# Optimization experiments

Measured on AMD Instinct MI355X. Metric: run time of the kernel, lower is better.

## Reference

```python
import jax, jax.numpy as jnp
import numpy as np

D_MODEL = 1024
D_HIDDEN = 4096
NUM_EXPERTS = 8
K_ACTIVE = 2


def setup_inputs() -> dict:
    key = jax.random.key(0)
    ks = jax.random.split(key, 8)
    x = jax.random.normal(ks[0], (1, 2048, D_MODEL), dtype=jnp.float32)
    gate_w = jax.random.normal(ks[1], (D_MODEL, NUM_EXPERTS), dtype=jnp.float32) * 0.02
    gate_b = jnp.zeros((NUM_EXPERTS,), dtype=jnp.float32)
    w1 = jax.random.normal(ks[2], (NUM_EXPERTS, D_MODEL, D_HIDDEN), dtype=jnp.float32) * 0.02
    b1 = jnp.zeros((NUM_EXPERTS, D_HIDDEN), dtype=jnp.float32)
    w2 = jax.random.normal(ks[3], (NUM_EXPERTS, D_HIDDEN, D_MODEL), dtype=jnp.float32) * 0.02
    b2 = jnp.zeros((NUM_EXPERTS, D_MODEL), dtype=jnp.float32)
    return {"x": x, "gate_w": gate_w, "gate_b": gate_b,
            "w1": w1, "b1": b1, "w2": w2, "b2": b2}


def reference(x, gate_w, gate_b, w1, b1, w2, b2):
    B, S, D = x.shape
    xf = x.reshape(-1, D)                                    # [T, D]
    logits = xf @ gate_w + gate_b                            # [T, E]
    top_w, top_idx = jax.lax.top_k(logits, K_ACTIVE)         # [T, K]
    top_w = jax.nn.softmax(top_w, axis=-1)                   # softmax over selected experts
    # combine-weight per expert: sum over k slots of one-hot(idx) * weight -> [T, E]
    gates = jnp.sum(jax.nn.one_hot(top_idx, NUM_EXPERTS, dtype=xf.dtype) * top_w[..., None], axis=1)
    # expert FFN applied per expert (dropout is identity in eval): gelu is exact (erf), matching torch nn.GELU default
    h = jax.nn.gelu(jnp.einsum('td,edh->teh', xf, w1) + b1[None], approximate=False)  # [T, E, H]
    y = jnp.einsum('teh,ehd->ted', h, w2) + b2[None]         # [T, E, D]
    out = jnp.einsum('ted,te->td', y, gates)                 # weighted combine of selected experts
    return out.reshape(B, S, D)
```

## Files before the change

kernel.cpp:

```cpp
#include <hip/hip_runtime.h>
#include <stdint.h>

typedef unsigned short u16;
typedef __attribute__((ext_vector_type(8))) short s16x8;
typedef __attribute__((ext_vector_type(8))) u16  u16x8;
typedef __attribute__((ext_vector_type(4))) u16  u16x4;
typedef __attribute__((ext_vector_type(4))) float f32x4;

#define T_TOKENS 2048
#define DM 1024
#define DH 4096
#define NE 8
#define BK 64
#define PAD2 256
#define MAXS2 (T_TOKENS*2 + NE*PAD2)
#define RB1 (MAXS2/256)
#define RB2 (MAXS2/128)
#define BM 128
#define BN 128
#define MAXSLOTS (T_TOKENS*2 + NE*BM)
#define ROWBLK (MAXSLOTS/BM)

__device__ __forceinline__ u16 f2bf(float f) {
    union { float ff; uint32_t u; } v; v.ff = f;
    uint32_t r = v.u + 0x7fffu + ((v.u >> 16) & 1u);
    return (u16)(r >> 16);
}

#define GLOAD_LDS16(gsrc, ldst) \
    __builtin_amdgcn_global_load_lds((const __attribute__((address_space(1))) uint32_t*)(gsrc), \
                                     (__attribute__((address_space(3))) uint32_t*)(ldst), 16, 0, 0)

#define WAIT_VM8() asm volatile("s_waitcnt vmcnt(8)" ::: "memory")
#define WAIT_VM0() asm volatile("s_waitcnt vmcnt(0)" ::: "memory")

__global__ void k_convert(const float* __restrict__ x, u16* __restrict__ xbf,
                          int* __restrict__ ctrl) {
    int i = blockIdx.x * blockDim.x + threadIdx.x;
    const f32x4* xv = (const f32x4*)x;
    f32x4 a = xv[2*i], b = xv[2*i+1];
    u16x8 o;
    o[0]=f2bf(a[0]); o[1]=f2bf(a[1]); o[2]=f2bf(a[2]); o[3]=f2bf(a[3]);
    o[4]=f2bf(b[0]); o[5]=f2bf(b[1]); o[6]=f2bf(b[2]); o[7]=f2bf(b[3]);
    ((u16x8*)xbf)[i] = o;
    if (blockIdx.x == 0 && threadIdx.x < 32) ctrl[threadIdx.x] = 0;
}

__global__ void __launch_bounds__(256) k_transpose(const float* __restrict__ src,
                                                   u16* __restrict__ dst,
                                                   int K, int N, int nw0, int NW) {
    __shared__ float tile[64][65];
    const int e = blockIdx.z;
    const int n0 = nw0 + blockIdx.x * 64, k0 = blockIdx.y * 64;
    const float* s = src + (size_t)e * K * N;
    u16* d = dst + (size_t)e * K * NW;
    const int tx = threadIdx.x & 15, ty = threadIdx.x >> 4;
    #pragma unroll
    for (int j = 0; j < 4; ++j) {
        int r = ty * 4 + j;
        f32x4 v = *(const f32x4*)(s + (size_t)(k0 + r) * N + n0 + tx * 4);
        tile[r][tx*4+0] = v[0]; tile[r][tx*4+1] = v[1];
        tile[r][tx*4+2] = v[2]; tile[r][tx*4+3] = v[3];
    }
    __syncthreads();
    #pragma unroll
    for (int j = 0; j < 4; ++j) {
        int n = ty * 4 + j;
        u16x4 w;
        #pragma unroll
        for (int c = 0; c < 4; ++c) w[c] = f2bf(tile[tx*4+c][n]);
        *(u16x4*)(d + (size_t)(n0 - nw0 + n) * K + k0 + tx * 4) = w;
    }
}

__global__ void __launch_bounds__(64) k_gate(const float* __restrict__ x,
                                             const float* __restrict__ gw,
                                             const float* __restrict__ gb,
                                             int* __restrict__ cnt,
                                             int* __restrict__ tt_idx,
                                             float* __restrict__ tt_w) {
    const int t = blockIdx.x;
    const int lane = threadIdx.x;
    float acc[NE] = {0.f,0.f,0.f,0.f,0.f,0.f,0.f,0.f};
    const float* xr = x + (size_t)t * DM;
    #pragma unroll
    for (int c = 0; c < DM/64; ++c) {
        float xv = xr[lane + 64*c];
        const float* g = gw + (size_t)(lane + 64*c) * NE;
        #pragma unroll
        for (int e = 0; e < NE; ++e) acc[e] += xv * g[e];
    }
    #pragma unroll
    for (int e = 0; e < NE; ++e) {
        #pragma unroll
        for (int off = 32; off >= 1; off >>= 1)
            acc[e] += __shfl_xor(acc[e], off, 64);
    }
    if (lane == 0) {
        float l[NE];
        #pragma unroll
        for (int e = 0; e < NE; ++e) l[e] = acc[e] + gb[e];
        int i0 = 0;
        #pragma unroll
        for (int e = 1; e < NE; ++e) if (l[e] > l[i0]) i0 = e;
        int i1 = (i0 == 0) ? 1 : 0;
        #pragma unroll
        for (int e = 0; e < NE; ++e) if (e != i0 && l[e] > l[i1]) i1 = e;
        float m  = l[i0];
        float w0 = expf(l[i0] - m), w1 = expf(l[i1] - m);
        float s = w0 + w1; w0 /= s; w1 /= s;
        tt_idx[t*2] = i0; tt_idx[t*2+1] = i1;
        tt_w[t*2] = w0;  tt_w[t*2+1] = w1;
        atomicAdd(&cnt[i0], 1); atomicAdd(&cnt[i1], 1);
    }
}

__global__ void k_offsets(const int* __restrict__ cnt, int* __restrict__ fill,
                          int* __restrict__ off, int pad) {
    if (threadIdx.x == 0 && blockIdx.x == 0) {
        int a = 0;
        for (int e = 0; e < NE; ++e) {
            off[e] = a;
            a += (cnt[e] + pad - 1) / pad * pad;
            fill[e] = 0;
        }
        off[NE] = a;
    }
}

__global__ void k_scatter(const int* __restrict__ tt_idx, const float* __restrict__ tt_w,
                          const int* __restrict__ off, int* __restrict__ fill,
                          int* __restrict__ slot_token, float* __restrict__ slot_gate) {
    int t = blockIdx.x * blockDim.x + threadIdx.x;
    if (t >= T_TOKENS) return;
    #pragma unroll
    for (int k = 0; k < 2; ++k) {
        int e = tt_idx[t*2+k];
        int pos = off[e] + atomicAdd(&fill[e], 1);
        slot_token[pos] = t;
        slot_gate[pos]  = tt_w[t*2+k];
    }
}

__device__ __forceinline__ void mma64(const u16* As, const u16* Bs, int lane,
                                      int wr, int wc, f32x4 acc[4][4]) {
    #pragma unroll
    for (int ko = 0; ko < 2; ++ko) {
        s16x8 af[4], bfr[4];
        #pragma unroll
        for (int m = 0; m < 4; ++m) {
            int row = wr*64 + m*16 + (lane & 15);
            int sl = (ko*4 + (lane >> 4)) ^ (row & 7);
            af[m] = *(const s16x8*)&As[row*BK + sl*8];
        }
        #pragma unroll
        for (int n = 0; n < 4; ++n) {
            int col = wc*64 + n*16 + (lane & 15);
            int sl = (ko*4 + (lane >> 4)) ^ (col & 7);
            bfr[n] = *(const s16x8*)&Bs[col*BK + sl*8];
        }
        #pragma unroll
        for (int m = 0; m < 4; ++m)
            #pragma unroll
            for (int n = 0; n < 4; ++n)
                acc[m][n] = __builtin_amdgcn_mfma_f32_16x16x32_bf16(af[m], bfr[n], acc[m][n], 0, 0, 0);
    }
}

__device__ __forceinline__ void mma256(const u16* As, const u16* Bs, int lane,
                                       int wr, int wc, f32x4 acc[8][4]) {
    #pragma unroll
    for (int ko = 0; ko < 2; ++ko) {
        s16x8 af[8], bfr[4];
        #pragma unroll
        for (int m = 0; m < 8; ++m) {
            int row = wr*128 + m*16 + (lane & 15);
            int sl = (ko*4 + (lane >> 4)) ^ (row & 7);
            af[m] = *(const s16x8*)&As[row*BK + sl*8];
        }
        #pragma unroll
        for (int n = 0; n < 4; ++n) {
            int col = wc*64 + n*16 + (lane & 15);
            int sl = (ko*4 + (lane >> 4)) ^ (col & 7);
            bfr[n] = *(const s16x8*)&Bs[col*BK + sl*8];
        }
        #pragma unroll
        for (int m = 0; m < 8; ++m)
            #pragma unroll
            for (int n = 0; n < 4; ++n)
                acc[m][n] = __builtin_amdgcn_mfma_f32_16x16x32_bf16(af[m], bfr[n], acc[m][n], 0, 0, 0);
    }
}

__global__ void __launch_bounds__(512, 2) k_ffn1_256(
    const u16* __restrict__ xbf, const u16* __restrict__ wt,
    const float* __restrict__ b1, const int* __restrict__ slot_token,
    const int* __restrict__ off, u16* __restrict__ h, int cb0, int NW)
{
    __shared__ u16 As[2][256*BK];
    __shared__ u16 Bs[2][256*BK];
    const int rb = blockIdx.y, cbl = blockIdx.x;
    const int total = off[NE];
    const int r0 = rb * 256;
    if (r0 >= total) return;
    int e = 0;
    while (e < NE-1 && off[e+1] <= r0) e++;
    const u16* Bsrc = wt + (size_t)e * DM * NW;
    const float* be = b1 + (size_t)e * DH;
    const int colbase = (cb0 + cbl) * 256;

    const int tid = threadIdx.x;
    const int lane = tid & 63, wid = tid >> 6;
    const int wr = wid >> 2, wc = wid & 3;

    const u16* gA[4]; const u16* gB[4];
    #pragma unroll
    for (int i = 0; i < 4; ++i) {
        int row = wid*32 + i*8 + (lane >> 3);
        int g = (lane & 7) ^ (row & 7);
        int tok = slot_token[r0 + row];
        gA[i] = xbf + (size_t)tok * DM + g*8;
        gB[i] = Bsrc + (size_t)(cbl*256 + row) * DM + g*8;
    }

    f32x4 acc[8][4];
    #pragma unroll
    for (int m = 0; m < 8; ++m)
        #pragma unroll
        for (int n = 0; n < 4; ++n) acc[m][n] = (f32x4){0.f,0.f,0.f,0.f};

    #define STG1(buf, kt) do {                                                \
        _Pragma("unroll")                                                     \
        for (int i = 0; i < 4; ++i) {                                         \
            GLOAD_LDS16(gA[i] + (kt)*BK, &As[buf][(wid*32 + i*8)*BK]);        \
            GLOAD_LDS16(gB[i] + (kt)*BK, &Bs[buf][(wid*32 + i*8)*BK]);        \
        }                                                                     \
    } while (0)

    const int NT = DM / BK;
    STG1(0, 0);
    STG1(1, 1);
    #pragma unroll 1
    for (int kt = 0; kt < NT; ++kt) {
        if (kt + 1 < NT) WAIT_VM8(); else WAIT_VM0();
        __builtin_amdgcn_s_barrier();
        __builtin_amdgcn_s_setprio(1);
        mma256(As[kt & 1], Bs[kt & 1], lane, wr, wc, acc);
        __builtin_amdgcn_s_setprio(0);
        __builtin_amdgcn_s_barrier();
        if (kt + 2 < NT) STG1(kt & 1, kt + 2);
    }
    #undef STG1

    #pragma unroll
    for (int n = 0; n < 4; ++n) {
        int col = colbase + wc*64 + n*16 + (lane & 15);
        float bb = be[col];
        #pragma unroll
        for (int m = 0; m < 8; ++m) {
            int rbase = r0 + wr*128 + m*16 + (lane >> 4)*4;
            #pragma unroll
            for (int i = 0; i < 4; ++i) {
                float v = acc[m][n][i] + bb;
                float gv = 0.5f * v * (1.0f + erff(v * 0.70710678118654752f));
                h[(size_t)(rbase + i)*DH + col] = f2bf(gv);
            }
        }
    }
}

__global__ void __launch_bounds__(256) k_ffn2_b16(
    const u16* __restrict__ h, const u16* __restrict__ w2t,
    const float* __restrict__ b2, const int* __restrict__ slot_token,
    const float* __restrict__ slot_gate, const int* __restrict__ off,
    float* __restrict__ out)
{
    __shared__ u16 As[2][BM*BK];
    __shared__ u16 Bs[2][BN*BK];
    const int rb = blockIdx.y, cb = blockIdx.x;
    const int total = off[NE];
    const int r0 = rb * BM;
    if (r0 >= total) return;
    int e = 0;
    while (e < NE-1 && off[e+1] <= r0) e++;
    const u16* Bsrc = w2t + (size_t)e * DH * DM;
    const float* be = b2 + (size_t)e * DM;

    const int tid = threadIdx.x;
    const int lane = tid & 63, wid = tid >> 6;
    const int wr = wid >> 1, wc = wid & 1;

    const u16* gA[4]; const u16* gB[4];
    #pragma unroll
    for (int i = 0; i < 4; ++i) {
        int row = wid*32 + i*8 + (lane >> 3);
        int g = (lane & 7) ^ (row & 7);
        gA[i] = h + (size_t)(r0 + row) * DH + g*8;
        gB[i] = Bsrc + (size_t)(cb*BN + row) * DH + g*8;
    }

    f32x4 acc[4][4];
    #pragma unroll
    for (int m = 0; m < 4; ++m)
        #pragma unroll
        for (int n = 0; n < 4; ++n) acc[m][n] = (f32x4){0.f,0.f,0.f,0.f};

    #define STG2(buf, kt) do {                                                \
        _Pragma("unroll")                                                     \
        for (int i = 0; i < 4; ++i) {                                         \
            GLOAD_LDS16(gA[i] + (kt)*BK, &As[buf][(wid*32 + i*8)*BK]);        \
            GLOAD_LDS16(gB[i] + (kt)*BK, &Bs[buf][(wid*32 + i*8)*BK]);        \
        }                                                                     \
    } while (0)

    const int NT = DH / BK;
    STG2(0, 0);
    STG2(1, 1);
    #pragma unroll 1
    for (int kt = 0; kt < NT; ++kt) {
        if (kt + 1 < NT) WAIT_VM8(); else WAIT_VM0();
        __builtin_amdgcn_s_barrier();
        __builtin_amdgcn_s_setprio(1);
        mma64(As[kt & 1], Bs[kt & 1], lane, wr, wc, acc);
        __builtin_amdgcn_s_setprio(0);
        __builtin_amdgcn_s_barrier();
        if (kt + 2 < NT) STG2(kt & 1, kt + 2);
    }
    #undef STG2

    float bb[4];
    #pragma unroll
    for (int n = 0; n < 4; ++n) bb[n] = be[cb*BN + wc*64 + n*16 + (lane & 15)];
    #pragma unroll
    for (int m = 0; m < 4; ++m) {
        #pragma unroll
        for (int i = 0; i < 4; ++i) {
            int s = r0 + wr*64 + m*16 + (lane >> 4)*4 + i;
            int tok = slot_token[s];
            float g = slot_gate[s];
            if (g != 0.0f) {
                float* orow = out + (size_t)tok * DM + cb*BN + wc*64;
                #pragma unroll
                for (int n = 0; n < 4; ++n)
                    atomicAdd(orow + n*16 + (lane & 15), g * (acc[m][n][i] + bb[n]));
            }
        }
    }
}


__global__ void __launch_bounds__(256) k_ffn1_f32(
    const u16* __restrict__ xbf, const float* __restrict__ w1,
    const float* __restrict__ b1, const int* __restrict__ slot_token,
    const int* __restrict__ off, u16* __restrict__ h)
{
    __shared__ u16 As[BM*BK];
    __shared__ u16 Bs[BN*BK];
    const int rb = blockIdx.y, cb = blockIdx.x;
    const int total = off[NE];
    const int r0 = rb * BM;
    if (r0 >= total) return;
    int e = 0;
    while (e < NE-1 && off[e+1] <= r0) e++;
    const float* Bsrc = w1 + (size_t)e * DM * DH;
    const float* be   = b1 + (size_t)e * DH;

    const int tid = threadIdx.x;
    const int lane = tid & 63, wid = tid >> 6;
    const int wr = wid >> 1, wc = wid & 1;

    const u16* gA[4];
    #pragma unroll
    for (int i = 0; i < 4; ++i) {
        int row = wid*32 + i*8 + (lane >> 3);
        int g = (lane & 7) ^ (row & 7);
        int tok = slot_token[r0 + row];
        gA[i] = xbf + (size_t)tok * DM + g*8;
    }
    const int tc = tid & 31, tr = tid >> 5;
    const float* gB = Bsrc + (size_t)(tr*8) * DH + cb*BN + tc*4;

    f32x4 acc[4][4];
    #pragma unroll
    for (int m = 0; m < 4; ++m)
        #pragma unroll
        for (int n = 0; n < 4; ++n) acc[m][n] = (f32x4){0.f,0.f,0.f,0.f};

    for (int kt = 0; kt < DM/BK; ++kt) {
        #pragma unroll
        for (int i = 0; i < 4; ++i)
            GLOAD_LDS16(gA[i] + kt*BK, &As[(wid*32 + i*8)*BK]);
        f32x4 bv[8];
        #pragma unroll
        for (int j = 0; j < 8; ++j)
            bv[j] = *(const f32x4*)(gB + (size_t)(kt*BK + j) * DH);
        #pragma unroll
        for (int c = 0; c < 4; ++c) {
            int n = tc*4 + c;
            int sl = tr ^ (n & 7);
            s16x8 pk;
            #pragma unroll
            for (int j = 0; j < 8; ++j) pk[j] = (short)f2bf(bv[j][c]);
            *(s16x8*)&Bs[n*BK + sl*8] = pk;
        }
        __syncthreads();
        mma64(As, Bs, lane, wr, wc, acc);
        __syncthreads();
    }
    #pragma unroll
    for (int n = 0; n < 4; ++n) {
        int col = cb*BN + wc*64 + n*16 + (lane & 15);
        float bb = be[col];
        #pragma unroll
        for (int m = 0; m < 4; ++m) {
            int rbase = r0 + wr*64 + m*16 + (lane >> 4)*4;
            #pragma unroll
            for (int i = 0; i < 4; ++i) {
                float v = acc[m][n][i] + bb;
                float gv = 0.5f * v * (1.0f + erff(v * 0.70710678118654752f));
                h[(size_t)(rbase + i)*DH + col] = f2bf(gv);
            }
        }
    }
}

__global__ void __launch_bounds__(256) k_ffn2_f32(
    const u16* __restrict__ h, const float* __restrict__ w2,
    const float* __restrict__ b2, const int* __restrict__ slot_token,
    const float* __restrict__ slot_gate, const int* __restrict__ off,
    float* __restrict__ out)
{
    __shared__ u16 As[BM*BK];
    __shared__ u16 Bs[BN*BK];
    const int rb = blockIdx.y, cb = blockIdx.x;
    const int total = off[NE];
    const int r0 = rb * BM;
    if (r0 >= total) return;
    int e = 0;
    while (e < NE-1 && off[e+1] <= r0) e++;
    const float* Bsrc = w2 + (size_t)e * DH * DM;
    const float* be   = b2 + (size_t)e * DM;

    const int tid = threadIdx.x;
    const int lane = tid & 63, wid = tid >> 6;
    const int wr = wid >> 1, wc = wid & 1;

    const u16* gA[4];
    #pragma unroll
    for (int i = 0; i < 4; ++i) {
        int row = wid*32 + i*8 + (lane >> 3);
        int g = (lane & 7) ^ (row & 7);
        gA[i] = h + (size_t)(r0 + row) * DH + g*8;
    }
    const int tc = tid & 31, tr = tid >> 5;
    const float* gB = Bsrc + (size_t)(tr*8) * DM + cb*BN + tc*4;

    f32x4 acc[4][4];
    #pragma unroll
    for (int m = 0; m < 4; ++m)
        #pragma unroll
        for (int n = 0; n < 4; ++n) acc[m][n] = (f32x4){0.f,0.f,0.f,0.f};

    for (int kt = 0; kt < DH/BK; ++kt) {
        #pragma unroll
        for (int i = 0; i < 4; ++i)
            GLOAD_LDS16(gA[i] + kt*BK, &As[(wid*32 + i*8)*BK]);
        f32x4 bv[8];
        #pragma unroll
        for (int j = 0; j < 8; ++j)
            bv[j] = *(const f32x4*)(gB + (size_t)(kt*BK + j) * DM);
        #pragma unroll
        for (int c = 0; c < 4; ++c) {
            int n = tc*4 + c;
            int sl = tr ^ (n & 7);
            s16x8 pk;
            #pragma unroll
            for (int j = 0; j < 8; ++j) pk[j] = (short)f2bf(bv[j][c]);
            *(s16x8*)&Bs[n*BK + sl*8] = pk;
        }
        __syncthreads();
        mma64(As, Bs, lane, wr, wc, acc);
        __syncthreads();
    }
    float bb[4];
    #pragma unroll
    for (int n = 0; n < 4; ++n) bb[n] = be[cb*BN + wc*64 + n*16 + (lane & 15)];
    #pragma unroll
    for (int m = 0; m < 4; ++m) {
        #pragma unroll
        for (int i = 0; i < 4; ++i) {
            int s = r0 + wr*64 + m*16 + (lane >> 4)*4 + i;
            int tok = slot_token[s];
            float g = slot_gate[s];
            if (g != 0.0f) {
                float* orow = out + (size_t)tok * DM + cb*BN + wc*64;
                #pragma unroll
                for (int n = 0; n < 4; ++n)
                    atomicAdd(orow + n*16 + (lane & 15), g * (acc[m][n][i] + bb[n]));
            }
        }
    }
}

extern "C" void kernel_launch(void* const* d_in, const int* in_sizes, int n_in,
                              void* d_out, int out_size, void* d_ws, size_t ws_size,
                              hipStream_t stream)
{
    (void)in_sizes; (void)n_in; (void)out_size;
    const float* x  = (const float*)d_in[0];
    const float* gw = (const float*)d_in[1];
    const float* gb = (const float*)d_in[2];
    const float* w1 = (const float*)d_in[3];
    const float* b1 = (const float*)d_in[4];
    const float* w2 = (const float*)d_in[5];
    const float* b2 = (const float*)d_in[6];
    float* out = (float*)d_out;
    char* ws = (char*)d_ws;

    const size_t OFF_XBF = 0;
    const size_t OFF_H   = 4194304;
    const size_t OFF_ST  = OFF_H + (size_t)MAXS2 * DH * 2;
    const size_t OFF_SG  = OFF_ST + MAXS2 * 4;
    const size_t OFF_TI  = OFF_SG + MAXS2 * 4;
    const size_t OFF_TW  = OFF_TI + T_TOKENS * 2 * 4;
    const size_t OFF_CT  = OFF_TW + T_TOKENS * 2 * 4;
    const size_t OFF_WT  = (OFF_CT + 128 + 255) & ~(size_t)255;
    const size_t NEED_FULL = OFF_WT + (size_t)NE * DM * DH * 2;
    const size_t NEED_HALF = OFF_WT + (size_t)NE * DM * (DH/2) * 2;

    if (ws_size >= NEED_HALF) {
        u16*   xbf        = (u16*)(ws + OFF_XBF);
        u16*   h          = (u16*)(ws + OFF_H);
        int*   slot_token = (int*)(ws + OFF_ST);
        float* slot_gate  = (float*)(ws + OFF_SG);
        int*   tt_idx     = (int*)(ws + OFF_TI);
        float* tt_w       = (float*)(ws + OFF_TW);
        int*   ctrl       = (int*)(ws + OFF_CT);
        u16*   wt         = (u16*)(ws + OFF_WT);
        int* cnt = ctrl; int* fill = ctrl + 8; int* offs = ctrl + 16;
        const int full = (ws_size >= NEED_FULL);

        hipMemsetAsync(slot_token, 0, 2 * MAXS2 * 4, stream);
        hipMemsetAsync(out, 0, (size_t)T_TOKENS * DM * sizeof(float), stream);

        k_convert<<<(T_TOKENS*DM/8 + 255)/256, 256, 0, stream>>>(x, xbf, ctrl);
        k_gate<<<T_TOKENS, 64, 0, stream>>>(x, gw, gb, cnt, tt_idx, tt_w);
        k_offsets<<<1, 64, 0, stream>>>(cnt, fill, offs, PAD2);
        k_scatter<<<(T_TOKENS + 255)/256, 256, 0, stream>>>(tt_idx, tt_w, offs, fill,
                                                            slot_token, slot_gate);
        if (full) {
            k_transpose<<<dim3(DH/64, DM/64, NE), 256, 0, stream>>>(w1, wt, DM, DH, 0, DH);
            k_ffn1_256<<<dim3(DH/256, RB1), 512, 0, stream>>>(xbf, wt, b1, slot_token, offs, h, 0, DH);
        } else {
            k_transpose<<<dim3(DH/128, DM/64, NE), 256, 0, stream>>>(w1, wt, DM, DH, 0, DH/2);
            k_ffn1_256<<<dim3(DH/512, RB1), 512, 0, stream>>>(xbf, wt, b1, slot_token, offs, h, 0, DH/2);
            k_transpose<<<dim3(DH/128, DM/64, NE), 256, 0, stream>>>(w1, wt, DM, DH, DH/2, DH/2);
            k_ffn1_256<<<dim3(DH/512, RB1), 512, 0, stream>>>(xbf, wt, b1, slot_token, offs, h, DH/512, DH/2);
        }
        k_transpose<<<dim3(DM/64, DH/64, NE), 256, 0, stream>>>(w2, wt, DH, DM, 0, DM);
        k_ffn2_b16<<<dim3(DM/BN, RB2), 256, 0, stream>>>(h, wt, b2, slot_token, slot_gate, offs, out);
    } else {
        u16*   xbf        = (u16*)(ws);
        u16*   h          = (u16*)(ws + 4194304);
        int*   slot_token = (int*)(ws + 46137344);
        float* slot_gate  = (float*)(ws + 46157824);
        int*   tt_idx     = (int*)(ws + 46178304);
        float* tt_w       = (float*)(ws + 46194688);
        int*   ctrl       = (int*)(ws + 46211072);
        int* cnt = ctrl; int* fill = ctrl + 8; int* offs = ctrl + 16;

        hipMemsetAsync(slot_token, 0, 2 * MAXSLOTS * 4, stream);
        hipMemsetAsync(out, 0, (size_t)T_TOKENS * DM * sizeof(float), stream);

        k_convert<<<(T_TOKENS*DM/8 + 255)/256, 256, 0, stream>>>(x, xbf, ctrl);
        k_gate<<<T_TOKENS, 64, 0, stream>>>(x, gw, gb, cnt, tt_idx, tt_w);
        k_offsets<<<1, 64, 0, stream>>>(cnt, fill, offs, BM);
        k_scatter<<<(T_TOKENS + 255)/256, 256, 0, stream>>>(tt_idx, tt_w, offs, fill,
                                                            slot_token, slot_gate);
        k_ffn1_f32<<<dim3(DH/BN, ROWBLK), 256, 0, stream>>>(xbf, w1, b1, slot_token, offs, h);
        k_ffn2_f32<<<dim3(DM/BN, ROWBLK), 256, 0, stream>>>(h, w2, b2, slot_token, slot_gate, offs, out);
    }
}
```

Before: 343.5 us.

## Shrink FFN1 tile to 256x128 single-buffered with higher occupancy

Replaces the 256x256 double-buffered FFN1 GEMM with a 256x128 tile, single LDS buffer, and plain syncthreads around each k-step, raising the occupancy hint to 4 blocks per CU. This trades the explicit prefetch pipeline and larger per-block reuse for smaller LDS and register footprint, more blocks, and more concurrent waves to hide memory latency. It loses the overlap of global loads with MFMA inside a block and rereads the A tile twice as often.

```diff
diff --git a/kernel.cpp b/kernel.cpp
--- a/kernel.cpp
+++ b/kernel.cpp
@@ -167,38 +167,13 @@
     }
 }
 
-__device__ __forceinline__ void mma256(const u16* As, const u16* Bs, int lane,
-                                       int wr, int wc, f32x4 acc[8][4]) {
-    #pragma unroll
-    for (int ko = 0; ko < 2; ++ko) {
-        s16x8 af[8], bfr[4];
-        #pragma unroll
-        for (int m = 0; m < 8; ++m) {
-            int row = wr*128 + m*16 + (lane & 15);
-            int sl = (ko*4 + (lane >> 4)) ^ (row & 7);
-            af[m] = *(const s16x8*)&As[row*BK + sl*8];
-        }
-        #pragma unroll
-        for (int n = 0; n < 4; ++n) {
-            int col = wc*64 + n*16 + (lane & 15);
-            int sl = (ko*4 + (lane >> 4)) ^ (col & 7);
-            bfr[n] = *(const s16x8*)&Bs[col*BK + sl*8];
-        }
-        #pragma unroll
-        for (int m = 0; m < 8; ++m)
-            #pragma unroll
-            for (int n = 0; n < 4; ++n)
-                acc[m][n] = __builtin_amdgcn_mfma_f32_16x16x32_bf16(af[m], bfr[n], acc[m][n], 0, 0, 0);
-    }
-}
-
-__global__ void __launch_bounds__(512, 2) k_ffn1_256(
+__global__ void __launch_bounds__(512, 4) k_ffn1_b16(
     const u16* __restrict__ xbf, const u16* __restrict__ wt,
     const float* __restrict__ b1, const int* __restrict__ slot_token,
     const int* __restrict__ off, u16* __restrict__ h, int cb0, int NW)
 {
-    __shared__ u16 As[2][256*BK];
-    __shared__ u16 Bs[2][256*BK];
+    __shared__ u16 As[256*BK];
+    __shared__ u16 Bs[128*BK];
     const int rb = blockIdx.y, cbl = blockIdx.x;
     const int total = off[NE];
     const int r0 = rb * 256;
@@ -207,58 +182,54 @@
     while (e < NE-1 && off[e+1] <= r0) e++;
     const u16* Bsrc = wt + (size_t)e * DM * NW;
     const float* be = b1 + (size_t)e * DH;
-    const int colbase = (cb0 + cbl) * 256;
+    const int colbase = (cb0 + cbl) * 128;
 
     const int tid = threadIdx.x;
     const int lane = tid & 63, wid = tid >> 6;
-    const int wr = wid >> 2, wc = wid & 3;
-
-    const u16* gA[4]; const u16* gB[4];
+    const int wr = wid >> 1, wc = wid & 1;
+
+    const u16* gA[4]; const u16* gB[2];
     #pragma unroll
     for (int i = 0; i < 4; ++i) {
         int row = wid*32 + i*8 + (lane >> 3);
         int g = (lane & 7) ^ (row & 7);
         int tok = slot_token[r0 + row];
         gA[i] = xbf + (size_t)tok * DM + g*8;
-        gB[i] = Bsrc + (size_t)(cbl*256 + row) * DM + g*8;
-    }
-
-    f32x4 acc[8][4];
-    #pragma unroll
-    for (int m = 0; m < 8; ++m)
+    }
+    #pragma unroll
+    for (int i = 0; i < 2; ++i) {
+        int n = wid*16 + i*8 + (lane >> 3);
+        int g = (lane & 7) ^ (n & 7);
+        gB[i] = Bsrc + (size_t)(cbl*128 + n) * DM + g*8;
+    }
+
+    f32x4 acc[4][4];
+    #pragma unroll
+    for (int m = 0; m < 4; ++m)
         #pragma unroll
         for (int n = 0; n < 4; ++n) acc[m][n] = (f32x4){0.f,0.f,0.f,0.f};
 
-    #define STG1(buf, kt) do {                                                \
-        _Pragma("unroll")                                                     \
-        for (int i = 0; i < 4; ++i) {                                         \
-            GLOAD_LDS16(gA[i] + (kt)*BK, &As[buf][(wid*32 + i*8)*BK]);        \
-            GLOAD_LDS16(gB[i] + (kt)*BK, &Bs[buf][(wid*32 + i*8)*BK]);        \
-        }                                                                     \
-    } while (0)
-
     const int NT = DM / BK;
-    STG1(0, 0);
-    STG1(1, 1);
     #pragma unroll 1
     for (int kt = 0; kt < NT; ++kt) {
-        if (kt + 1 < NT) WAIT_VM8(); else WAIT_VM0();
-        __builtin_amdgcn_s_barrier();
-        __builtin_amdgcn_s_setprio(1);
-        mma256(As[kt & 1], Bs[kt & 1], lane, wr, wc, acc);
-        __builtin_amdgcn_s_setprio(0);
-        __builtin_amdgcn_s_barrier();
-        if (kt + 2 < NT) STG1(kt & 1, kt + 2);
-    }
-    #undef STG1
+        #pragma unroll
+        for (int i = 0; i < 4; ++i)
+            GLOAD_LDS16(gA[i] + kt*BK, &As[(wid*32 + i*8)*BK]);
+        #pragma unroll
+        for (int i = 0; i < 2; ++i)
+            GLOAD_LDS16(gB[i] + kt*BK, &Bs[(wid*16 + i*8)*BK]);
+        __syncthreads();
+        mma64(As, Bs, lane, wr, wc, acc);
+        __syncthreads();
+    }
 
     #pragma unroll
     for (int n = 0; n < 4; ++n) {
         int col = colbase + wc*64 + n*16 + (lane & 15);
         float bb = be[col];
         #pragma unroll
-        for (int m = 0; m < 8; ++m) {
-            int rbase = r0 + wr*128 + m*16 + (lane >> 4)*4;
+        for (int m = 0; m < 4; ++m) {
+            int rbase = r0 + wr*64 + m*16 + (lane >> 4)*4;
             #pragma unroll
             for (int i = 0; i < 4; ++i) {
                 float v = acc[m][n][i] + bb;
@@ -550,12 +521,12 @@
                                                             slot_token, slot_gate);
         if (full) {
             k_transpose<<<dim3(DH/64, DM/64, NE), 256, 0, stream>>>(w1, wt, DM, DH, 0, DH);
-            k_ffn1_256<<<dim3(DH/256, RB1), 512, 0, stream>>>(xbf, wt, b1, slot_token, offs, h, 0, DH);
+            k_ffn1_b16<<<dim3(DH/128, RB1), 512, 0, stream>>>(xbf, wt, b1, slot_token, offs, h, 0, DH);
         } else {
             k_transpose<<<dim3(DH/128, DM/64, NE), 256, 0, stream>>>(w1, wt, DM, DH, 0, DH/2);
-            k_ffn1_256<<<dim3(DH/512, RB1), 512, 0, stream>>>(xbf, wt, b1, slot_token, offs, h, 0, DH/2);
+            k_ffn1_b16<<<dim3(DH/256, RB1), 512, 0, stream>>>(xbf, wt, b1, slot_token, offs, h, 0, DH/2);
             k_transpose<<<dim3(DH/128, DM/64, NE), 256, 0, stream>>>(w1, wt, DM, DH, DH/2, DH/2);
-            k_ffn1_256<<<dim3(DH/512, RB1), 512, 0, stream>>>(xbf, wt, b1, slot_token, offs, h, DH/512, DH/2);
+            k_ffn1_b16<<<dim3(DH/256, RB1), 512, 0, stream>>>(xbf, wt, b1, slot_token, offs, h, DH/256, DH/2);
         }
         k_transpose<<<dim3(DM/64, DH/64, NE), 256, 0, stream>>>(w2, wt, DH, DM, 0, DM);
         k_ffn2_b16<<<dim3(DM/BN, RB2), 256, 0, stream>>>(h, wt, b2, slot_token, slot_gate, offs, out);
```

New measurement: 307.0 us. -10.7%, faster.
